# Optimization experiments

Hardware: AMD Instinct MI355X
Metric: run time of the kernel (lower is better)

## Reference

```python
import jax, jax.numpy as jnp
import numpy as np

B, S, D, H = 2, 2048, 1024, 16
DK = D // H


def setup_inputs() -> dict:
    key = jax.random.key(0)
    ks = jax.random.split(key, 11)
    sd = 1.0 / np.sqrt(D)  # torch Linear default init scale (uniform bound)
    def lin(k):
        kw, kb = jax.random.split(k)
        W = jax.random.uniform(kw, (D, D), jnp.float32, -sd, sd)
        b = jax.random.uniform(kb, (D,), jnp.float32, -sd, sd)
        return W, b
    Wq, bq = lin(ks[0]); Wk, bk = lin(ks[1]); Wv, bv = lin(ks[2]); Wo, bo = lin(ks[3])
    return {
        "Q": jax.random.normal(ks[4], (B, S, D), jnp.float32),
        "K": jax.random.normal(ks[5], (B, S, D), jnp.float32),
        "V": jax.random.normal(ks[6], (B, S, D), jnp.float32),
        "mask": jnp.ones((B, S), jnp.int32),
        "Wq": Wq, "bq": bq, "Wk": Wk, "bk": bk,
        "Wv": Wv, "bv": bv, "Wo": Wo, "bo": bo,
    }


def reference(Q, K, V, mask, Wq, bq, Wk, bk, Wv, bv, Wo, bo):
    b, s, _ = Q.shape
    # projections (torch Linear: x @ W.T + b), split heads -> [b, h, s, dk]
    def proj(x, W, bias):
        return (x @ W.T + bias).reshape(b, -1, H, DK).transpose(0, 2, 1, 3)
    q = proj(Q, Wq, bq)
    k = proj(K, Wk, bk)
    v = proj(V, Wv, bv)
    scores = jnp.einsum('bhqd,bhkd->bhqk', q, k) / jnp.sqrt(jnp.float32(DK))
    m = mask[:, None, None, :]  # [b,1,1,s_k]
    scores = jnp.where(m == 0, jnp.float32(-jnp.inf), scores)
    attn = jax.nn.softmax(scores, axis=-1)
    out = jnp.einsum('bhqk,bhkd->bhqd', attn, v)
    out = out.transpose(0, 2, 1, 3).reshape(b, s, H * DK)
    return out @ Wo.T + bo
```

## Files before the change

### kernel.cpp

```cpp
#include <hip/hip_runtime.h>
#include <stdint.h>

#define BB 2
#define HH 16
#define SS 2048
#define DKK 64
#define DD 1024
#define TT (BB * SS)

typedef __attribute__((ext_vector_type(8))) short bf16x8;
typedef __attribute__((ext_vector_type(4))) float f32x4;
typedef __attribute__((ext_vector_type(16))) float f32x16;

static __device__ __forceinline__ unsigned short f2bf(float f) {
  union { float f; uint32_t u; } c; c.f = f;
  return (unsigned short)((c.u + 0x7FFFu + ((c.u >> 16) & 1u)) >> 16);
}

static __device__ __forceinline__ f32x4 zero4() {
  f32x4 z; z[0] = 0.f; z[1] = 0.f; z[2] = 0.f; z[3] = 0.f; return z;
}
static __device__ __forceinline__ f32x16 zero16() {
  f32x16 z;
#pragma unroll
  for (int i = 0; i < 16; ++i) z[i] = 0.f;
  return z;
}

static __device__ __forceinline__ uint32_t cvt_pk_bf16(float lo, float hi) {
  uint32_t r;
  asm("v_cvt_pk_bf16_f32 %0, %1, %2" : "=v"(r) : "v"(lo), "v"(hi));
  return r;
}

static __device__ __forceinline__ uint32_t xswap_u32(uint32_t v) {
  return (uint32_t)__shfl_xor((int)v, 32);
}
static __device__ __forceinline__ float xhalf_sum(float x) {
  return x + __shfl_xor(x, 32);
}

static __device__ __forceinline__ void gload_lds16(const void* g, void* l) {
  __builtin_amdgcn_global_load_lds(
      (const __attribute__((address_space(1))) void*)g,
      (__attribute__((address_space(3))) void*)l, 16, 0, 0);
}

static __device__ __forceinline__ int swz(int row, int col) {
  return ((((col >> 3) ^ row) & 7) << 3) | (col & 7);
}

struct CvtArgs {
  const float* src[4];
  unsigned short* dst[4];
  int n4[4];
};

__global__ __launch_bounds__(256) void cvt_all(CvtArgs a) {
  const int id = blockIdx.y;
  const float4* s = (const float4*)a.src[id];
  ushort4* d = (ushort4*)a.dst[id];
  const int n4 = a.n4[id];
  for (int i = blockIdx.x * blockDim.x + threadIdx.x; i < n4;
       i += gridDim.x * blockDim.x) {
    float4 v = s[i];
    ushort4 o;
    o.x = f2bf(v.x); o.y = f2bf(v.y); o.z = f2bf(v.z); o.w = f2bf(v.w);
    d[i] = o;
  }
}

struct GemmJob {
  const void* A;
  const unsigned short* W;
  const float* bias;
  void* out;
  int mode;
  float scale;
};
struct GemmArgs { GemmJob job[3]; };

template <int BM, int NBUF, bool AFP32>
__global__ __launch_bounds__(256) void gemm_kernel(GemmArgs args) {
  constexpr int MI = BM / 32;
  __shared__ __align__(16) unsigned short As[NBUF][BM][64];
  __shared__ __align__(16) unsigned short Bs[NBUF][128][64];
  const GemmJob jb = args.job[blockIdx.z];
  const int tid = threadIdx.x;
  const int lane = tid & 63;
  const int wv = tid >> 6;
  const int fr = lane & 15, fq = lane >> 4;
  const int wr = (wv >> 1) * (BM / 2), wc = (wv & 1) * 64;

  const int nb = gridDim.x * gridDim.y;
  const int bid = blockIdx.y * gridDim.x + blockIdx.x;
  const int virt = (bid & 7) * (nb >> 3) + (bid >> 3);
  const int n0 = (virt & 7) * 128, m0 = (virt >> 3) * BM;

  const int lrow = lane >> 3;
  const int lchunk = (lane & 7) ^ lrow;
  const unsigned short* __restrict__ Ab = (const unsigned short*)jb.A;
  const float* __restrict__ A32 = (const float*)jb.A;
  const unsigned short* __restrict__ W = jb.W;

  f32x4 acc[MI][4];
#pragma unroll
  for (int i = 0; i < MI; ++i)
#pragma unroll
    for (int j = 0; j < 4; ++j) acc[i][j] = zero4();

  constexpr int SEGA_W = BM / 32;
  constexpr int NT = DD / 64;

  float4 ra0[SEGA_W], ra1[SEGA_W];

  auto load_a = [&](int k0) {
    if constexpr (AFP32) {
#pragma unroll
      for (int i = 0; i < SEGA_W; ++i) {
        const int seg = wv * SEGA_W + i;
        const int row = seg * 8 + lrow;
        const float* sp = A32 + (size_t)(m0 + row) * DD + k0 + lchunk * 8;
        ra0[i] = *(const float4*)sp;
        ra1[i] = *(const float4*)(sp + 4);
      }
    }
  };
  auto write_a = [&](int buf) {
    if constexpr (AFP32) {
#pragma unroll
      for (int i = 0; i < SEGA_W; ++i) {
        const int seg = wv * SEGA_W + i;
        uint4 wdat;
        wdat.x = cvt_pk_bf16(ra0[i].x, ra0[i].y);
        wdat.y = cvt_pk_bf16(ra0[i].z, ra0[i].w);
        wdat.z = cvt_pk_bf16(ra1[i].x, ra1[i].y);
        wdat.w = cvt_pk_bf16(ra1[i].z, ra1[i].w);
        *(uint4*)((char*)&As[buf][0][0] + seg * 1024 + lane * 16) = wdat;
      }
    }
  };
  auto stage_a_gl = [&](int buf, int k0) {
    if constexpr (!AFP32) {
#pragma unroll
      for (int i = 0; i < SEGA_W; ++i) {
        const int seg = wv * SEGA_W + i;
        const int row = seg * 8 + lrow;
        gload_lds16(Ab + (size_t)(m0 + row) * DD + k0 + lchunk * 8,
                    (char*)&As[buf][0][0] + seg * 1024);
      }
    }
  };
  auto stage_w = [&](int buf, int k0) {
#pragma unroll
    for (int i = 0; i < 4; ++i) {
      const int seg = wv * 4 + i;
      const int row = seg * 8 + lrow;
      gload_lds16(W + (size_t)(n0 + row) * DD + k0 + lchunk * 8,
                  (char*)&Bs[buf][0][0] + seg * 1024);
    }
  };

  int cur = 0;
  load_a(0);
  write_a(0);
  stage_a_gl(0, 0);
  stage_w(0, 0);

  for (int t = 0; t < NT; ++t) {
    __syncthreads();
    if (t + 1 < NT) {
      load_a((t + 1) * 64);
      stage_a_gl(cur ^ 1, (t + 1) * 64);
      stage_w(cur ^ 1, (t + 1) * 64);
    }
#pragma unroll
    for (int kk = 0; kk < 2; ++kk) {
      bf16x8 af[MI], bfr[4];
#pragma unroll
      for (int i = 0; i < MI; ++i) {
        const int r = wr + i * 16 + fr;
        af[i] = *(const bf16x8*)&As[cur][r][swz(r, kk * 32 + fq * 8)];
      }
#pragma unroll
      for (int j = 0; j < 4; ++j) {
        const int r = wc + j * 16 + fr;
        bfr[j] = *(const bf16x8*)&Bs[cur][r][swz(r, kk * 32 + fq * 8)];
      }
      __builtin_amdgcn_s_setprio(1);
#pragma unroll
      for (int i = 0; i < MI; ++i)
#pragma unroll
        for (int j = 0; j < 4; ++j)
          acc[i][j] = __builtin_amdgcn_mfma_f32_16x16x32_bf16(af[i], bfr[j],
                                                              acc[i][j], 0, 0, 0);
      __builtin_amdgcn_s_setprio(0);
    }
    if (t + 1 < NT) write_a(cur ^ 1);
    cur ^= 1;
  }

  const int mode = jb.mode;
  const float scale = jb.scale;
  if (mode == 1) {
    float* out = (float*)jb.out;
#pragma unroll
    for (int i = 0; i < MI; ++i)
#pragma unroll
      for (int j = 0; j < 4; ++j) {
        const int col = n0 + wc + j * 16 + fr;
        const float bv = jb.bias[col];
#pragma unroll
        for (int r = 0; r < 4; ++r) {
          const int row = m0 + wr + i * 16 + fq * 4 + r;
          out[(size_t)row * DD + col] = (acc[i][j][r] + bv) * scale;
        }
      }
  } else if (mode == 0) {
    unsigned short* out = (unsigned short*)jb.out;
#pragma unroll
    for (int i = 0; i < MI; ++i)
#pragma unroll
      for (int j = 0; j < 4; ++j) {
        const int col = n0 + wc + j * 16 + fr;
        const float bv = jb.bias[col];
        const int h = col >> 6, dk = col & 63;
#pragma unroll
        for (int r = 0; r < 4; ++r) {
          const int row = m0 + wr + i * 16 + fq * 4 + r;
          const int b = row >> 11, s = row & (SS - 1);
          out[(((size_t)(b * HH + h)) * SS + s) * DKK + dk] =
              f2bf((acc[i][j][r] + bv) * scale);
        }
      }
  } else {
    unsigned short* out = (unsigned short*)jb.out;
#pragma unroll
    for (int i = 0; i < MI; ++i)
#pragma unroll
      for (int j = 0; j < 4; ++j) {
        const int col = n0 + wc + j * 16 + fr;
        const float bv = jb.bias[col];
        const int h = col >> 6, dk = col & 63;
#pragma unroll
        for (int r = 0; r < 4; ++r) {
          const int row = m0 + wr + i * 16 + fq * 4 + r;
          const int b = row >> 11, s = row & (SS - 1);
          out[(((size_t)(b * HH + h)) * DKK + dk) * SS + s] =
              f2bf((acc[i][j][r] + bv) * scale);
        }
      }
  }
}

__global__ __launch_bounds__(512, 2) void attn_kernel(
    const unsigned short* __restrict__ qh, const unsigned short* __restrict__ kh,
    const unsigned short* __restrict__ vt, const int* __restrict__ maskp,
    unsigned short* __restrict__ ao) {
  __shared__ __align__(16) char smem[65536];

  const int tid = threadIdx.x;
  const int lane = tid & 63, wv = tid >> 6;
  const int lo = lane & 31, hi = lane >> 5;
  const int g = wv >> 2, qw = wv & 3;

  const int bid = blockIdx.x;
  const int virt = (bid & 7) * 32 + (bid >> 3);
  const int bh = virt >> 3, qblk = virt & 7;
  const int bB = bh >> 4, h = bh & 15;
  const int q0 = qblk * 256;
  const size_t base = (size_t)bh * SS * DKK;
  const size_t vbase = (size_t)bh * DKK * SS;

  const int lrow = lane >> 3;
  const int lchunk = (lane & 7) ^ lrow;
  const int srow = wv * 8 + lrow;

  bf16x8 aq[2][4];
#pragma unroll
  for (int st = 0; st < 2; ++st) {
    const int qrow = q0 + qw * 64 + st * 32 + lo;
#pragma unroll
    for (int tt = 0; tt < 4; ++tt)
      aq[st][tt] =
          *(const bf16x8*)(qh + base + (size_t)qrow * DKK + 16 * tt + hi * 8);
  }

  float lsum[2] = {0.f, 0.f};
  f32x16 o[2][2];
#pragma unroll
  for (int st = 0; st < 2; ++st) {
    o[st][0] = zero16();
    o[st][1] = zero16();
  }

  const int kvb = g * (SS / 2);
  constexpr int NTH = SS / 128;

  uint32_t okbits = 0;
  for (int t = 0; t < NTH; ++t) {
    const int mv = maskp[bB * SS + kvb + t * 64 + lane];
    okbits |= (__all(mv != 0)) ? (1u << t) : 0u;
  }

#define STAGE(d, t)                                                           \
  {                                                                           \
    const int ka = (t) * 64, kb2 = SS / 2 + (t) * 64;                         \
    gload_lds16(kh + base + (size_t)(ka + srow) * DKK + lchunk * 8,           \
                smem + ((d)) * 8192 + wv * 1024);                             \
    gload_lds16(vt + vbase + (size_t)srow * SS + ka + lchunk * 8,             \
                smem + 32768 + ((d)) * 8192 + wv * 1024);                     \
    gload_lds16(kh + base + (size_t)(kb2 + srow) * DKK + lchunk * 8,          \
                smem + (2 + (d)) * 8192 + wv * 1024);                         \
    gload_lds16(vt + vbase + (size_t)srow * SS + kb2 + lchunk * 8,            \
                smem + 32768 + (2 + (d)) * 8192 + wv * 1024);                 \
  }

  STAGE(0, 0);
  int cur = 0;

  for (int t = 0; t < NTH; ++t) {
    __syncthreads();
    if (t + 1 < NTH) STAGE(cur ^ 1, t + 1);
    const bool ok = (okbits >> t) & 1;

    const unsigned short* Ksb =
        (const unsigned short*)(smem + (g * 2 + cur) * 8192);
    const unsigned short* Vsb =
        (const unsigned short*)(smem + 32768 + (g * 2 + cur) * 8192);

    f32x16 sc[2][2];
#pragma unroll
    for (int st = 0; st < 2; ++st) { sc[st][0] = zero16(); sc[st][1] = zero16(); }
    __builtin_amdgcn_s_setprio(1);
#pragma unroll
    for (int tt = 0; tt < 4; ++tt) {
      bf16x8 k0 = *(const bf16x8*)&Ksb[lo * 64 + swz(lo, (hi + 2 * tt) * 8)];
      bf16x8 k1 =
          *(const bf16x8*)&Ksb[(32 + lo) * 64 + swz(32 + lo, (hi + 2 * tt) * 8)];
#pragma unroll
      for (int st = 0; st < 2; ++st) {
        sc[st][0] =
            __builtin_amdgcn_mfma_f32_32x32x16_bf16(k0, aq[st][tt], sc[st][0], 0, 0, 0);
        sc[st][1] =
            __builtin_amdgcn_mfma_f32_32x32x16_bf16(k1, aq[st][tt], sc[st][1], 0, 0, 0);
      }
    }
    __builtin_amdgcn_s_setprio(0);

    if (!ok) {
      const int mt = maskp[bB * SS + kvb + t * 64 + lane];
#pragma unroll
      for (int r = 0; r < 16; ++r) {
        const int kvi = (r & 3) + 8 * (r >> 2) + 4 * hi;
        const float a0 = (__shfl(mt, kvi) != 0) ? 0.f : -1e30f;
        const float a1 = (__shfl(mt, 32 + kvi) != 0) ? 0.f : -1e30f;
#pragma unroll
        for (int st = 0; st < 2; ++st) {
          sc[st][0][r] += a0;
          sc[st][1][r] += a1;
        }
      }
    }

    bf16x8 pb[2][4];
#pragma unroll
    for (int st = 0; st < 2; ++st) {
#pragma unroll
      for (int r = 0; r < 16; ++r) {
        sc[st][0][r] = __builtin_amdgcn_exp2f(sc[st][0][r]);
        sc[st][1][r] = __builtin_amdgcn_exp2f(sc[st][1][r]);
      }
      float t8[8];
#pragma unroll
      for (int i = 0; i < 8; ++i)
        t8[i] = (sc[st][0][2 * i] + sc[st][0][2 * i + 1]) +
                (sc[st][1][2 * i] + sc[st][1][2 * i + 1]);
      lsum[st] += ((t8[0] + t8[1]) + (t8[2] + t8[3])) +
                  ((t8[4] + t8[5]) + (t8[6] + t8[7]));

#pragma unroll
      for (int kb = 0; kb < 2; ++kb) {
#pragma unroll
        for (int tt = 0; tt < 2; ++tt) {
          const int b = tt * 8;
          uint32_t a0 = cvt_pk_bf16(sc[st][kb][b + 0], sc[st][kb][b + 1]);
          uint32_t a1 = cvt_pk_bf16(sc[st][kb][b + 2], sc[st][kb][b + 3]);
          uint32_t a2 = cvt_pk_bf16(sc[st][kb][b + 4], sc[st][kb][b + 5]);
          uint32_t a3 = cvt_pk_bf16(sc[st][kb][b + 6], sc[st][kb][b + 7]);
          const uint32_t e0 = xswap_u32(hi ? a0 : a2);
          const uint32_t e1 = xswap_u32(hi ? a1 : a3);
          union { uint32_t w[4]; bf16x8 v; } u;
          u.w[0] = hi ? e0 : a0;
          u.w[1] = hi ? e1 : a1;
          u.w[2] = hi ? a2 : e0;
          u.w[3] = hi ? a3 : e1;
          pb[st][kb * 2 + tt] = u.v;
        }
      }
    }

    __builtin_amdgcn_s_setprio(1);
#pragma unroll
    for (int tt = 0; tt < 4; ++tt) {
      bf16x8 v0 = *(const bf16x8*)&Vsb[lo * 64 + swz(lo, (hi + 2 * tt) * 8)];
      bf16x8 v1 =
          *(const bf16x8*)&Vsb[(32 + lo) * 64 + swz(32 + lo, (hi + 2 * tt) * 8)];
#pragma unroll
      for (int st = 0; st < 2; ++st) {
        o[st][0] = __builtin_amdgcn_mfma_f32_32x32x16_bf16(v0, pb[st][tt], o[st][0], 0, 0, 0);
        o[st][1] = __builtin_amdgcn_mfma_f32_32x32x16_bf16(v1, pb[st][tt], o[st][1], 0, 0, 0);
      }
    }
    __builtin_amdgcn_s_setprio(0);

    cur ^= 1;
  }
#undef STAGE

  lsum[0] = xhalf_sum(lsum[0]);
  lsum[1] = xhalf_sum(lsum[1]);

  float* mb = (float*)smem;
#pragma unroll
  for (int st = 0; st < 2; ++st) {
    const int rec = (qw * 64 + lane) * 33;
    __syncthreads();
    if (g == 1) {
      mb[rec] = lsum[st];
#pragma unroll
      for (int i = 0; i < 16; ++i) {
        mb[rec + 1 + i] = o[st][0][i];
        mb[rec + 17 + i] = o[st][1][i];
      }
    }
    __syncthreads();
    if (g == 0) {
      const float inv = 1.f / (lsum[st] + mb[rec]);
      const int token = bB * SS + q0 + qw * 64 + st * 32 + lo;
      unsigned short* aop = ao + (size_t)token * DD + h * DKK;
#pragma unroll
      for (int db = 0; db < 2; ++db) {
#pragma unroll
        for (int gq = 0; gq < 4; ++gq) {
          const int rb = rec + 1 + db * 16 + 4 * gq;
          float c0 = (o[st][db][4 * gq + 0] + mb[rb + 0]) * inv;
          float c1 = (o[st][db][4 * gq + 1] + mb[rb + 1]) * inv;
          float c2 = (o[st][db][4 * gq + 2] + mb[rb + 2]) * inv;
          float c3 = (o[st][db][4 * gq + 3] + mb[rb + 3]) * inv;
          uint2 w;
          w.x = cvt_pk_bf16(c0, c1);
          w.y = cvt_pk_bf16(c2, c3);
          *(uint2*)&aop[db * 32 + 8 * gq + 4 * hi] = w;
        }
      }
    }
  }
}

extern "C" void kernel_launch(void* const* d_in, const int* in_sizes, int n_in,
                              void* d_out, int out_size, void* d_ws, size_t ws_size,
                              hipStream_t stream) {
  const float* Q = (const float*)d_in[0];
  const float* K = (const float*)d_in[1];
  const float* V = (const float*)d_in[2];
  const int* mask = (const int*)d_in[3];
  const float* Wq = (const float*)d_in[4];
  const float* bq = (const float*)d_in[5];
  const float* Wk = (const float*)d_in[6];
  const float* bk = (const float*)d_in[7];
  const float* Wv = (const float*)d_in[8];
  const float* bv = (const float*)d_in[9];
  const float* Wo = (const float*)d_in[10];
  const float* bo = (const float*)d_in[11];

  char* ws = (char*)d_ws;
  const size_t SZ_X = (size_t)TT * DD * 2;
  const size_t SZ_W = (size_t)DD * DD * 2;
  unsigned short* Wqb = (unsigned short*)(ws + 0 * SZ_W);
  unsigned short* Wkb = (unsigned short*)(ws + 1 * SZ_W);
  unsigned short* Wvb = (unsigned short*)(ws + 2 * SZ_W);
  unsigned short* Wob = (unsigned short*)(ws + 3 * SZ_W);
  unsigned short* qh = (unsigned short*)(ws + 4 * SZ_W + 0 * SZ_X);
  unsigned short* kh = (unsigned short*)(ws + 4 * SZ_W + 1 * SZ_X);
  unsigned short* vt = (unsigned short*)(ws + 4 * SZ_W + 2 * SZ_X);
  unsigned short* ao = (unsigned short*)(ws + 4 * SZ_W + 3 * SZ_X);

  CvtArgs ca;
  ca.src[0] = Wq; ca.dst[0] = Wqb; ca.n4[0] = DD * DD / 4;
  ca.src[1] = Wk; ca.dst[1] = Wkb; ca.n4[1] = DD * DD / 4;
  ca.src[2] = Wv; ca.dst[2] = Wvb; ca.n4[2] = DD * DD / 4;
  ca.src[3] = Wo; ca.dst[3] = Wob; ca.n4[3] = DD * DD / 4;
  cvt_all<<<dim3(512, 4), 256, 0, stream>>>(ca);

  const float SCALE_Q = 0.125f * 1.44269504088896f;

  GemmArgs ga;
  ga.job[0] = {Q, Wqb, bq, qh, 0, SCALE_Q};
  ga.job[1] = {K, Wkb, bk, kh, 0, 1.0f};
  ga.job[2] = {V, Wvb, bv, vt, 2, 1.0f};
  gemm_kernel<64, 2, true><<<dim3(DD / 128, TT / 64, 3), 256, 0, stream>>>(ga);

  attn_kernel<<<dim3((TT / 256) * HH), 512, 0, stream>>>(qh, kh, vt, mask, ao);

  GemmArgs gf;
  gf.job[0] = {ao, Wob, bo, d_out, 1, 1.0f};
  gf.job[1] = gf.job[0];
  gf.job[2] = gf.job[0];
  gemm_kernel<64, 2, false><<<dim3(DD / 128, TT / 64, 1), 256, 0, stream>>>(gf);
}
```

Baseline: 114.5 us.

## Software-pipeline PV matmul one tile behind QK and split K/V staging

Restructures the attention loop so each iteration's P·V MFMAs use the previous tile's probabilities, interleaved right after the current QK^T MFMAs. The aim is to overlap the exp/convert softmax work with matrix-core work. K and V loads are now staged separately, and V is prefetched after a second barrier once the previous V buffer has been consumed. The change adds a __syncthreads per iteration, keeps pb live across iterations (more register pressure), and needs an epilogue for the final tile.

```diff
diff --git a/kernel.cpp b/kernel.cpp
--- a/kernel.cpp
+++ b/kernel.cpp
@@ -303,31 +303,36 @@
     okbits |= (__all(mv != 0)) ? (1u << t) : 0u;
   }
 
-#define STAGE(d, t)                                                           \
+#define STAGE_K(d, t)                                                         \
   {                                                                           \
     const int ka = (t) * 64, kb2 = SS / 2 + (t) * 64;                         \
     gload_lds16(kh + base + (size_t)(ka + srow) * DKK + lchunk * 8,           \
                 smem + ((d)) * 8192 + wv * 1024);                             \
+    gload_lds16(kh + base + (size_t)(kb2 + srow) * DKK + lchunk * 8,          \
+                smem + (2 + (d)) * 8192 + wv * 1024);                         \
+  }
+#define STAGE_V(d, t)                                                         \
+  {                                                                           \
+    const int ka = (t) * 64, kb2 = SS / 2 + (t) * 64;                         \
     gload_lds16(vt + vbase + (size_t)srow * SS + ka + lchunk * 8,             \
                 smem + 32768 + ((d)) * 8192 + wv * 1024);                     \
-    gload_lds16(kh + base + (size_t)(kb2 + srow) * DKK + lchunk * 8,          \
-                smem + (2 + (d)) * 8192 + wv * 1024);                         \
     gload_lds16(vt + vbase + (size_t)srow * SS + kb2 + lchunk * 8,            \
                 smem + 32768 + (2 + (d)) * 8192 + wv * 1024);                 \
   }
 
-  STAGE(0, 0);
-  int cur = 0;
+  STAGE_K(0, 0);
+  STAGE_V(0, 0);
+
+  bf16x8 pb[2][4];
 
   for (int t = 0; t < NTH; ++t) {
+    const int cur = t & 1;
     __syncthreads();
-    if (t + 1 < NTH) STAGE(cur ^ 1, t + 1);
+    if (t + 1 < NTH) STAGE_K(cur ^ 1, t + 1);
     const bool ok = (okbits >> t) & 1;
 
     const unsigned short* Ksb =
         (const unsigned short*)(smem + (g * 2 + cur) * 8192);
-    const unsigned short* Vsb =
-        (const unsigned short*)(smem + 32768 + (g * 2 + cur) * 8192);
 
     f32x16 sc[2][2];
 #pragma unroll
@@ -346,7 +351,28 @@
             __builtin_amdgcn_mfma_f32_32x32x16_bf16(k1, aq[st][tt], sc[st][1], 0, 0, 0);
       }
     }
+
+    if (t > 0) {
+      const unsigned short* Vsb_p =
+          (const unsigned short*)(smem + 32768 + (g * 2 + (cur ^ 1)) * 8192);
+#pragma unroll
+      for (int tt = 0; tt < 4; ++tt) {
+        bf16x8 v0 = *(const bf16x8*)&Vsb_p[lo * 64 + swz(lo, (hi + 2 * tt) * 8)];
+        bf16x8 v1 = *(const bf16x8*)&Vsb_p[(32 + lo) * 64 +
+                                           swz(32 + lo, (hi + 2 * tt) * 8)];
+#pragma unroll
+        for (int st = 0; st < 2; ++st) {
+          o[st][0] = __builtin_amdgcn_mfma_f32_32x32x16_bf16(v0, pb[st][tt],
+                                                             o[st][0], 0, 0, 0);
+          o[st][1] = __builtin_amdgcn_mfma_f32_32x32x16_bf16(v1, pb[st][tt],
+                                                             o[st][1], 0, 0, 0);
+        }
+      }
+    }
     __builtin_amdgcn_s_setprio(0);
+
+    __syncthreads();
+    if (t + 1 < NTH) STAGE_V(cur ^ 1, t + 1);
 
     if (!ok) {
       const int mt = maskp[bB * SS + kvb + t * 64 + lane];
@@ -363,7 +389,6 @@
       }
     }
 
-    bf16x8 pb[2][4];
 #pragma unroll
     for (int st = 0; st < 2; ++st) {
 #pragma unroll
@@ -399,7 +424,11 @@
         }
       }
     }
-
+  }
+
+  {
+    const unsigned short* Vsb =
+        (const unsigned short*)(smem + 32768 + (g * 2 + ((NTH - 1) & 1)) * 8192);
     __builtin_amdgcn_s_setprio(1);
 #pragma unroll
     for (int tt = 0; tt < 4; ++tt) {
@@ -413,10 +442,9 @@
       }
     }
     __builtin_amdgcn_s_setprio(0);
-
-    cur ^= 1;
-  }
-#undef STAGE
+  }
+#undef STAGE_K
+#undef STAGE_V
 
   lsum[0] = xhalf_sum(lsum[0]);
   lsum[1] = xhalf_sum(lsum[1]);
```

Measured after the change: 118.5 us. +3.5%, slower.
